# Performance work log

Measured on AMD Instinct MI355X. Metric: run time of the kernel, lower is better.

Reference implementation:

```python
import jax, jax.numpy as jnp
import numpy as np

N = 50000      # nodes
E = 600000     # edges
DIN = 128
H1, H2, H3 = 128, 128, 64
EPS = 1e-5


def setup_inputs() -> dict:
    key = jax.random.key(0)
    ks = jax.random.split(key, 12)
    x = jax.random.normal(ks[0], (N, DIN), jnp.float32)
    edge_index = jax.random.randint(ks[1], (2, E), 0, N, dtype=jnp.int32).astype(jnp.int64)
    s = lambda f: np.float32(1.0 / np.sqrt(f))
    W1 = jax.random.normal(ks[2], (DIN, H1), jnp.float32) * s(DIN)
    b1 = jnp.zeros((H1,), jnp.float32)
    W2 = jax.random.normal(ks[3], (H1, H2), jnp.float32) * s(H1)
    b2 = jnp.zeros((H2,), jnp.float32)
    W3 = jax.random.normal(ks[4], (H2, H3), jnp.float32) * s(H2)
    b3 = jnp.zeros((H3,), jnp.float32)
    g1 = 1.0 + 0.1 * jax.random.normal(ks[5], (H1,), jnp.float32)
    be1 = 0.1 * jax.random.normal(ks[6], (H1,), jnp.float32)
    g2 = 1.0 + 0.1 * jax.random.normal(ks[7], (H2,), jnp.float32)
    be2 = 0.1 * jax.random.normal(ks[8], (H2,), jnp.float32)
    return {"x": x, "edge_index": edge_index, "W1": W1, "b1": b1, "g1": g1,
            "be1": be1, "W2": W2, "b2": b2, "g2": g2, "be2": be2,
            "W3": W3, "b3": b3}


def _gcn(h_in, W, b, src_sl, dst_sl, norm, n):
    # GCNConv: h = X W; out_i = sum_{j->i} norm_ij * h_j + b  (self-loops included)
    h = h_in @ W
    msg = h[src_sl] * norm[:, None]          # [E+N, F] gather + scale
    out = jax.ops.segment_sum(msg, dst_sl, num_segments=n)
    return out + b


def _bn(x, g, b):
    # training-mode BatchNorm1d over nodes (biased variance, eps=1e-5)
    m = x.mean(0)
    v = x.var(0)
    return g * (x - m) * jax.lax.rsqrt(v + EPS) + b


def reference(x, edge_index, W1, b1, g1, be1, W2, b2, g2, be2, W3, b3):
    src, dst = edge_index[0], edge_index[1]
    loops = jnp.arange(N, dtype=src.dtype)
    src_sl = jnp.concatenate([src, loops])
    dst_sl = jnp.concatenate([dst, loops])
    deg = jax.ops.segment_sum(jnp.ones_like(dst_sl, jnp.float32), dst_sl,
                              num_segments=N)
    dinv = jnp.where(deg > 0, jax.lax.rsqrt(deg), 0.0)
    norm = dinv[src_sl] * dinv[dst_sl]       # symmetric D^-1/2 (A+I) D^-1/2

    h = _gcn(x, W1, b1, src_sl, dst_sl, norm, N)
    h = jax.nn.relu(_bn(h, g1, be1))         # dropout is identity in eval mode
    h = _gcn(h, W2, b2, src_sl, dst_sl, norm, N)
    h = jax.nn.relu(_bn(h, g2, be2))
    out = _gcn(h, W3, b3, src_sl, dst_sl, norm, N)  # [N, 64]
    return out
```

## Files before the change

kernel.cpp:

```cpp
#include <hip/hip_runtime.h>
#include <hip/hip_bf16.h>


typedef __attribute__((ext_vector_type(8))) short short8;
typedef __attribute__((ext_vector_type(4))) float f32x4;

__device__ inline unsigned short f2bf(float f) {
    unsigned int u = __float_as_uint(f);
    return (unsigned short)((u + 0x7fff + ((u >> 16) & 1)) >> 16);
}
__device__ inline float bf2f_lo(unsigned int p) { return __uint_as_float(p << 16); }
__device__ inline float bf2f_hi(unsigned int p) { return __uint_as_float(p & 0xffff0000u); }

__device__ inline void bf4_acc(uint2 v, float* a) {
    a[0] += bf2f_lo(v.x); a[1] += bf2f_hi(v.x);
    a[2] += bf2f_lo(v.y); a[3] += bf2f_hi(v.y);
}

__global__ void prep_kernel(const int* __restrict__ dst, int E,
                            int* __restrict__ deg,
                            const float* __restrict__ x,
                            unsigned short* __restrict__ xb, int total4,
                            const float* __restrict__ W1,
                            const float* __restrict__ W2,
                            const float* __restrict__ W3,
                            unsigned short* __restrict__ wt1,
                            unsigned short* __restrict__ wt2,
                            unsigned short* __restrict__ wt3,
                            int EB, int XB) {
    const int b = blockIdx.x;
    const int t = threadIdx.x;
    if (b < EB) {
        int e = b * 256 + t;
        if (e < E) atomicAdd(deg + dst[e], 1);
    } else if (b < EB + XB) {
        int i = (b - EB) * 256 + t;
        if (i < total4) {
            float4 v = reinterpret_cast<const float4*>(x)[i];
            uint2 p;
            p.x = f2bf(v.x) | ((unsigned)f2bf(v.y) << 16);
            p.y = f2bf(v.z) | ((unsigned)f2bf(v.w) << 16);
            reinterpret_cast<uint2*>(xb)[i] = p;
        }
    } else if (b < EB + XB + 64) {
        int idx = (b - EB - XB) * 256 + t;
        int k = idx >> 7, nn = idx & 127;
        wt1[nn * 128 + k] = f2bf(W1[idx]);
    } else if (b < EB + XB + 128) {
        int idx = (b - EB - XB - 64) * 256 + t;
        int k = idx >> 7, nn = idx & 127;
        wt2[nn * 128 + k] = f2bf(W2[idx]);
    } else {
        int idx = (b - EB - XB - 128) * 256 + t;
        int k = idx >> 6, nn = idx & 63;
        wt3[nn * 128 + k] = f2bf(W3[idx]);
    }
}

__global__ __launch_bounds__(256) void prescan_kernel(
    const int* __restrict__ deg, int n, int B, float* __restrict__ dinv,
    int* __restrict__ bh, int* __restrict__ rowptr, int* __restrict__ bsum) {
    __shared__ int lh[64];
    __shared__ int sh[256];
    const int t = threadIdx.x, b = blockIdx.x;
    if (t < 64) lh[t] = 0;
    __syncthreads();
    const int base = b * 2048 + t * 8;
    int v[8];
    int run = 0;
#pragma unroll
    for (int j = 0; j < 8; ++j) {
        int idx = base + j;
        int d = 0;
        if (idx < n) {
            d = deg[idx];
            dinv[idx] = rsqrtf((float)(d + 1));
            atomicAdd(&lh[min(d, 63)], 1);
        }
        run += d;
        v[j] = run;
    }
    sh[t] = run;
    __syncthreads();
#pragma unroll
    for (int off = 1; off < 256; off <<= 1) {
        int add = (t >= off) ? sh[t - off] : 0;
        __syncthreads();
        sh[t] += add;
        __syncthreads();
    }
    int prev = (t > 0) ? sh[t - 1] : 0;
#pragma unroll
    for (int j = 0; j < 8; ++j) {
        int idx = base + j;
        if (idx < n) rowptr[idx + 1] = v[j] + prev;
    }
    if (t == 255) bsum[b] = sh[255];
    if (b == 0 && t == 0) rowptr[0] = 0;
    if (t < 64) bh[t * B + b] = lh[t];
}

__global__ void midscan_kernel(int* __restrict__ bh, int totalbh,
                               int* __restrict__ bsum, int B) {
    __shared__ int sh[256];
    const int t = threadIdx.x;
    int base = 0;
    for (int start = 0; start < totalbh; start += 256) {
        int i = start + t;
        int v = (i < totalbh) ? bh[i] : 0;
        sh[t] = v;
        __syncthreads();
#pragma unroll
        for (int off = 1; off < 256; off <<= 1) {
            int add = (t >= off) ? sh[t - off] : 0;
            __syncthreads();
            sh[t] += add;
            __syncthreads();
        }
        int excl = (t > 0 ? sh[t - 1] : 0) + base;
        if (i < totalbh) bh[i] = excl;
        base += sh[255];
        __syncthreads();
    }
    int v = (t < B) ? bsum[t] : 0;
    sh[t] = v;
    __syncthreads();
#pragma unroll
    for (int off = 1; off < 64; off <<= 1) {
        int add = (t >= off && t < 64) ? sh[t - off] : 0;
        __syncthreads();
        if (t < 64) sh[t] += add;
        __syncthreads();
    }
    if (t < B) bsum[t] = sh[t];
}

__global__ void place_scanC_kernel(const int* __restrict__ deg, int n, int B,
                                   const int* __restrict__ bh,
                                   const int* __restrict__ bsum,
                                   int* __restrict__ perm,
                                   int* __restrict__ rowptr) {
    const int t = threadIdx.x;
    if ((int)blockIdx.x < B) {
        const int b = blockIdx.x;
        __shared__ int lbase[64];
        __shared__ int lcur[64];
        if (t < 64) {
            lbase[t] = bh[t * B + b];
            lcur[t] = 0;
        }
        __syncthreads();
        const int lim = min((b + 1) * 2048, n);
        for (int i = b * 2048 + t; i < lim; i += 256) {
            int d = min(deg[i], 63);
            int r = atomicAdd(&lcur[d], 1);
            perm[lbase[d] + r] = i;
        }
    } else {
        const int c = blockIdx.x - B;
        if (c == 0) return;
        const int off = bsum[c - 1];
        const int lim = min((c + 1) * 2048, n);
        for (int i = c * 2048 + t; i < lim; i += 256) rowptr[i + 1] += off;
    }
}

__global__ void csr_build_kernel(const int* __restrict__ src,
                                 const int* __restrict__ dst, int E,
                                 int* __restrict__ rowptr,
                                 int* __restrict__ csr_src) {
    int e = blockIdx.x * blockDim.x + threadIdx.x;
    if (e < E) {
        int pos = atomicAdd(rowptr + dst[e], 1);
        csr_src[pos] = src[e];
    }
}

template <int NC, bool BN>
__global__ __launch_bounds__(256) void gemm_mfma(
    const unsigned short* __restrict__ A, const unsigned short* __restrict__ Wt,
    unsigned short* __restrict__ C, int n, const float* __restrict__ stats,
    const float* __restrict__ g, const float* __restrict__ be, float invn,
    const float* __restrict__ dinv) {
    __shared__ unsigned short Asd[64][136];
    __shared__ unsigned short Bsd[64][136];
    __shared__ float ssl[256];
    const int tid = threadIdx.x;
    const int wave = tid >> 6;
    const int lane = tid & 63;
    const int row0 = blockIdx.x * 64;
    const int col0 = blockIdx.y * 64;

    if (BN) {
        if (tid < 128) {
            float mean = stats[tid] * invn;
            float var = fmaf(-mean, mean, stats[128 + tid] * invn);
            float sc = g[tid] * rsqrtf(var + 1e-5f);
            ssl[tid] = sc;
            ssl[128 + tid] = fmaf(-mean, sc, be[tid]);
        }
        __syncthreads();
    }

    for (int idx = tid; idx < 64 * 16; idx += 256) {
        int r = idx >> 4;
        int c = (idx & 15) * 8;
        uint4 v = *reinterpret_cast<const uint4*>(Wt + (size_t)(col0 + r) * 128 + c);
        *reinterpret_cast<uint4*>(&Bsd[r][c]) = v;
    }
    for (int idx = tid; idx < 64 * 16; idx += 256) {
        int r = idx >> 4;
        int c = (idx & 15) * 8;
        int grow = row0 + r;
        uint4 v = make_uint4(0u, 0u, 0u, 0u);
        if (grow < n)
            v = *reinterpret_cast<const uint4*>(A + (size_t)grow * 128 + c);
        if (BN) {
            unsigned int p[4] = {v.x, v.y, v.z, v.w};
#pragma unroll
            for (int h = 0; h < 4; ++h) {
                int f = c + h * 2;
                float lo = fmaxf(fmaf(bf2f_lo(p[h]), ssl[f], ssl[128 + f]), 0.f);
                float hi = fmaxf(fmaf(bf2f_hi(p[h]), ssl[f + 1], ssl[129 + f]), 0.f);
                p[h] = f2bf(lo) | ((unsigned)f2bf(hi) << 16);
            }
            v = make_uint4(p[0], p[1], p[2], p[3]);
        }
        *reinterpret_cast<uint4*>(&Asd[r][c]) = v;
    }
    __syncthreads();

    f32x4 acc[4];
#pragma unroll
    for (int t = 0; t < 4; ++t) acc[t] = (f32x4)(0.f);

    const int l15 = lane & 15;
    const int quad = lane >> 4;
#pragma unroll
    for (int kb = 0; kb < 128; kb += 32) {
        short8 a = *reinterpret_cast<const short8*>(&Asd[wave * 16 + l15][kb + quad * 8]);
#pragma unroll
        for (int t = 0; t < 4; ++t) {
            short8 b = *reinterpret_cast<const short8*>(&Bsd[t * 16 + l15][kb + quad * 8]);
            acc[t] = __builtin_amdgcn_mfma_f32_16x16x32_bf16(a, b, acc[t], 0, 0, 0);
        }
    }

    const int rbase = row0 + wave * 16 + quad * 4;
    float dv[4] = {0.f, 0.f, 0.f, 0.f};
    if (rbase < n) {
        float4 d4 = *reinterpret_cast<const float4*>(dinv + rbase);
        dv[0] = d4.x; dv[1] = d4.y; dv[2] = d4.z; dv[3] = d4.w;
    }
#pragma unroll
    for (int t = 0; t < 4; ++t) {
        int col = col0 + t * 16 + l15;
#pragma unroll
        for (int r = 0; r < 4; ++r) {
            int row = rbase + r;
            if (row < n)
                C[(size_t)row * NC + col] = f2bf(acc[t][r] * dv[r]);
        }
    }
}

template <int F, bool STATS, bool OBF, bool SPLIT>
__global__ __launch_bounds__(256) void aggregate_kernel(
    const unsigned short* __restrict__ hs, const int* __restrict__ csr_src,
    const int* __restrict__ rowptr, const int* __restrict__ perm,
    const float* __restrict__ dinv, const float* __restrict__ bias,
    void* __restrict__ outp, int n, float* __restrict__ stats) {
    constexpr int FH = SPLIT ? (F / 2) : F;
    constexpr int LANES = FH / 4;
    constexpr int GROUPS = 256 / LANES;
    int wb = blockIdx.x;
    int nw = gridDim.x;
    int hb = 0;
    if (SPLIT) {
        const int xcd = wb & 7;
        hb = (xcd >= 4) ? (F / 2) : 0;
        wb = (wb >> 3) * 4 + (xcd & 3);
        nw = (nw >> 3) * 4;
    }
    const int lane = threadIdx.x % LANES;
    const int grp = threadIdx.x / LANES;
    const int fq = hb + lane * 4;
    const float4 b4 = *reinterpret_cast<const float4*>(bias + fq);
    float s[4] = {}, sq[4] = {};

    const int stride = nw * GROUPS * 4;

    for (int j0 = (wb * GROUPS + grp) * 4; j0 < n; j0 += stride) {
        const int nv = min(4, n - j0);
        int nd[4], e[4], end[4];
        float acc[4][4] = {};
#pragma unroll
        for (int q = 0; q < 4; ++q) {
            if (q < nv) {
                int node = perm[j0 + q];
                nd[q] = node;
                e[q] = (node == 0) ? 0 : rowptr[node - 1];
                end[q] = rowptr[node];
            } else {
                nd[q] = -1; e[q] = 0; end[q] = 0;
            }
        }
#pragma unroll
        for (int q = 0; q < 4; ++q)
            if (nd[q] >= 0)
                bf4_acc(*reinterpret_cast<const uint2*>(hs + (size_t)nd[q] * F + fq), acc[q]);
        int rem = end[0] - e[0];
#pragma unroll
        for (int q = 1; q < 4; ++q)
            if (q < nv) rem = min(rem, end[q] - e[q]);
        for (; rem >= 2; rem -= 2) {
            int i0[4], i1[4];
#pragma unroll
            for (int q = 0; q < 4; ++q) {
                i0[q] = csr_src[e[q]];
                i1[q] = csr_src[e[q] + 1];
                e[q] += 2;
            }
            uint2 v0[4], v1[4];
#pragma unroll
            for (int q = 0; q < 4; ++q) {
                v0[q] = *reinterpret_cast<const uint2*>(hs + (size_t)i0[q] * F + fq);
                v1[q] = *reinterpret_cast<const uint2*>(hs + (size_t)i1[q] * F + fq);
            }
#pragma unroll
            for (int q = 0; q < 4; ++q) {
                bf4_acc(v0[q], acc[q]);
                bf4_acc(v1[q], acc[q]);
            }
        }
#pragma unroll
        for (int q = 0; q < 4; ++q) {
            for (; e[q] < end[q]; ++e[q]) {
                int s0 = csr_src[e[q]];
                bf4_acc(*reinterpret_cast<const uint2*>(hs + (size_t)s0 * F + fq), acc[q]);
            }
        }
#pragma unroll
        for (int q = 0; q < 4; ++q) {
            if (nd[q] < 0) continue;
            const float di = dinv[nd[q]];
            float y[4];
            y[0] = fmaf(di, acc[q][0], b4.x);
            y[1] = fmaf(di, acc[q][1], b4.y);
            y[2] = fmaf(di, acc[q][2], b4.z);
            y[3] = fmaf(di, acc[q][3], b4.w);
            if (OBF) {
                uint2 p;
                p.x = f2bf(y[0]) | ((unsigned)f2bf(y[1]) << 16);
                p.y = f2bf(y[2]) | ((unsigned)f2bf(y[3]) << 16);
                *reinterpret_cast<uint2*>((unsigned short*)outp + (size_t)nd[q] * F + fq) = p;
            } else {
                *reinterpret_cast<float4*>((float*)outp + (size_t)nd[q] * F + fq) =
                    make_float4(y[0], y[1], y[2], y[3]);
            }
            if (STATS) {
#pragma unroll
                for (int j = 0; j < 4; ++j) {
                    s[j] += y[j];
                    sq[j] = fmaf(y[j], y[j], sq[j]);
                }
            }
        }
    }

    if (STATS) {
        __shared__ float sred[LANES][GROUPS + 1];
#pragma unroll
        for (int q = 0; q < 8; ++q) {
            float v = (q < 4) ? s[q] : sq[q - 4];
            sred[lane][grp] = v;
            __syncthreads();
            if (grp == 0) {
                float t = 0.f;
#pragma unroll
                for (int g = 0; g < GROUPS; ++g) t += sred[lane][g];
                int f = fq + (q & 3);
                atomicAdd(stats + ((q < 4) ? f : 128 + f), t);
            }
            __syncthreads();
        }
    }
}

extern "C" void kernel_launch(void* const* d_in, const int* in_sizes, int n_in,
                              void* d_out, int out_size, void* d_ws,
                              size_t ws_size, hipStream_t stream) {
    const float* x   = (const float*)d_in[0];
    const int*   ei  = (const int*)d_in[1];
    const float* W1  = (const float*)d_in[2];
    const float* b1  = (const float*)d_in[3];
    const float* g1  = (const float*)d_in[4];
    const float* be1 = (const float*)d_in[5];
    const float* W2  = (const float*)d_in[6];
    const float* b2  = (const float*)d_in[7];
    const float* g2  = (const float*)d_in[8];
    const float* be2 = (const float*)d_in[9];
    const float* W3  = (const float*)d_in[10];
    const float* b3  = (const float*)d_in[11];
    float* out = (float*)d_out;

    const int n = in_sizes[0] / 128;
    const int E = in_sizes[1] / 2;
    const int* src = ei;
    const int* dst = ei + E;

    const int B = (n + 2047) / 2048;

    float* wsf    = (float*)d_ws;
    float* stats1 = wsf;
    float* stats2 = stats1 + 256;
    int*   deg    = (int*)(stats2 + 256);
    float* dinv   = (float*)(deg + n);
    int*   bh     = (int*)(dinv + n + 64);
    int*   bsum   = bh + 64 * 32;
    int*   rowptr = bsum + 64;
    int*   perm   = rowptr + (n + 1);
    int*   csrsrc = perm + n;
    unsigned short* wt1 = (unsigned short*)(csrsrc + E);
    unsigned short* wt2 = wt1 + 128 * 128;
    unsigned short* wt3 = wt2 + 128 * 128;
    unsigned short* abuf = wt3 + 64 * 128;
    unsigned short* hsb  = abuf + (size_t)n * 128;

    const int EB = (E + 255) / 256;
    const int total4 = n * 32;
    const int XB = (total4 + 255) / 256;

    hipMemsetAsync(wsf, 0, (size_t)(512 + n) * 4, stream);
    prep_kernel<<<EB + XB + 160, 256, 0, stream>>>(dst, E, deg, x, abuf, total4,
                                                   W1, W2, W3, wt1, wt2, wt3,
                                                   EB, XB);
    prescan_kernel<<<B, 256, 0, stream>>>(deg, n, B, dinv, bh, rowptr, bsum);
    midscan_kernel<<<1, 256, 0, stream>>>(bh, 64 * B, bsum, B);
    place_scanC_kernel<<<2 * B, 256, 0, stream>>>(deg, n, B, bh, bsum, perm, rowptr);
    csr_build_kernel<<<EB, 256, 0, stream>>>(src, dst, E, rowptr, csrsrc);

    const int gemmRows = (n + 63) / 64;
    dim3 gemmGrid128(gemmRows, 2);
    dim3 gemmGrid64(gemmRows, 1);
    const int aggGrid = 512;
    const float invn = 1.0f / n;

    gemm_mfma<128, false><<<gemmGrid128, 256, 0, stream>>>(abuf, wt1, hsb, n, nullptr, nullptr, nullptr, invn, dinv);
    aggregate_kernel<128, true, true, true><<<aggGrid, 256, 0, stream>>>(hsb, csrsrc, rowptr, perm, dinv, b1, abuf, n, stats1);
    gemm_mfma<128, true><<<gemmGrid128, 256, 0, stream>>>(abuf, wt2, hsb, n, stats1, g1, be1, invn, dinv);
    aggregate_kernel<128, true, true, true><<<aggGrid, 256, 0, stream>>>(hsb, csrsrc, rowptr, perm, dinv, b2, abuf, n, stats2);
    gemm_mfma<64, true><<<gemmGrid64, 256, 0, stream>>>(abuf, wt3, hsb, n, stats2, g2, be2, invn, dinv);
    aggregate_kernel<64, false, false, false><<<aggGrid, 256, 0, stream>>>(hsb, csrsrc, rowptr, perm, dinv, b3, out, n, nullptr);
}
```

Before: 393.8 us.

## Partition CSR edges by source quarter and aggregate in grid-synchronized phases

Edges are bucketed per destination node by which quarter of the node range their source falls in, which builds a 4×-granular rowptr. The aggregation kernel then walks the four source quarters in separate phases separated by a software grid barrier. The aim is to keep each phase's gathered feature rows (about a quarter of the hidden matrix) resident in L2 and raise cache hit rates on the random gathers. In exchange it adds three grid-wide spin barriers per aggregation, which rely on all 512 blocks being co-resident. It also fixes a per-thread node count (MAXB=4) that only covers graphs up to a certain size, and makes the CSR build scans four times larger.

```diff
diff --git a/kernel.cpp b/kernel.cpp
--- a/kernel.cpp
+++ b/kernel.cpp
@@ -17,8 +17,9 @@
     a[2] += bf2f_lo(v.y); a[3] += bf2f_hi(v.y);
 }
 
-__global__ void prep_kernel(const int* __restrict__ dst, int E,
-                            int* __restrict__ deg,
+__global__ void prep_kernel(const int* __restrict__ src,
+                            const int* __restrict__ dst, int E, int qs,
+                            int* __restrict__ bc,
                             const float* __restrict__ x,
                             unsigned short* __restrict__ xb, int total4,
                             const float* __restrict__ W1,
@@ -32,7 +33,11 @@
     const int t = threadIdx.x;
     if (b < EB) {
         int e = b * 256 + t;
-        if (e < E) atomicAdd(deg + dst[e], 1);
+        if (e < E) {
+            int q = src[e] / qs;
+            if (q > 3) q = 3;
+            atomicAdd(bc + dst[e] * 4 + q, 1);
+        }
     } else if (b < EB + XB) {
         int i = (b - EB) * 256 + t;
         if (i < total4) {
@@ -57,28 +62,37 @@
     }
 }
 
-__global__ __launch_bounds__(256) void prescan_kernel(
-    const int* __restrict__ deg, int n, int B, float* __restrict__ dinv,
-    int* __restrict__ bh, int* __restrict__ rowptr, int* __restrict__ bsum) {
+__global__ __launch_bounds__(256) void prescan4_kernel(
+    const int* __restrict__ bc, int n, int B4, int* __restrict__ deg,
+    float* __restrict__ dinv, int* __restrict__ bh,
+    int* __restrict__ rowptr4, int* __restrict__ bsum4) {
     __shared__ int lh[64];
     __shared__ int sh[256];
     const int t = threadIdx.x, b = blockIdx.x;
+    const int n4 = n * 4;
     if (t < 64) lh[t] = 0;
     __syncthreads();
     const int base = b * 2048 + t * 8;
+    int c[8];
     int v[8];
     int run = 0;
 #pragma unroll
     for (int j = 0; j < 8; ++j) {
         int idx = base + j;
-        int d = 0;
-        if (idx < n) {
-            d = deg[idx];
-            dinv[idx] = rsqrtf((float)(d + 1));
+        c[j] = (idx < n4) ? bc[idx] : 0;
+        run += c[j];
+        v[j] = run;
+    }
+    const int node0 = base >> 2;
+#pragma unroll
+    for (int m = 0; m < 2; ++m) {
+        int node = node0 + m;
+        if (node < n) {
+            int d = c[m * 4] + c[m * 4 + 1] + c[m * 4 + 2] + c[m * 4 + 3];
+            deg[node] = d;
+            dinv[node] = rsqrtf((float)(d + 1));
             atomicAdd(&lh[min(d, 63)], 1);
         }
-        run += d;
-        v[j] = run;
     }
     sh[t] = run;
     __syncthreads();
@@ -93,15 +107,15 @@
 #pragma unroll
     for (int j = 0; j < 8; ++j) {
         int idx = base + j;
-        if (idx < n) rowptr[idx + 1] = v[j] + prev;
-    }
-    if (t == 255) bsum[b] = sh[255];
-    if (b == 0 && t == 0) rowptr[0] = 0;
-    if (t < 64) bh[t * B + b] = lh[t];
-}
-
-__global__ void midscan_kernel(int* __restrict__ bh, int totalbh,
-                               int* __restrict__ bsum, int B) {
+        if (idx < n4) rowptr4[idx + 1] = v[j] + prev;
+    }
+    if (t == 255) bsum4[b] = sh[255];
+    if (b == 0 && t == 0) rowptr4[0] = 0;
+    if (t < 64) bh[t * B4 + b] = lh[t];
+}
+
+__global__ void midscan4_kernel(int* __restrict__ bh, int totalbh,
+                                int* __restrict__ bsum4, int B4) {
     __shared__ int sh[256];
     const int t = threadIdx.x;
     int base = 0;
@@ -122,57 +136,232 @@
         base += sh[255];
         __syncthreads();
     }
-    int v = (t < B) ? bsum[t] : 0;
+    int v = (t < B4) ? bsum4[t] : 0;
     sh[t] = v;
     __syncthreads();
 #pragma unroll
-    for (int off = 1; off < 64; off <<= 1) {
-        int add = (t >= off && t < 64) ? sh[t - off] : 0;
-        __syncthreads();
-        if (t < 64) sh[t] += add;
-        __syncthreads();
-    }
-    if (t < B) bsum[t] = sh[t];
-}
-
-__global__ void place_scanC_kernel(const int* __restrict__ deg, int n, int B,
-                                   const int* __restrict__ bh,
-                                   const int* __restrict__ bsum,
-                                   int* __restrict__ perm,
-                                   int* __restrict__ rowptr) {
+    for (int off = 1; off < 256; off <<= 1) {
+        int add = (t >= off) ? sh[t - off] : 0;
+        __syncthreads();
+        sh[t] += add;
+        __syncthreads();
+    }
+    if (t < B4) bsum4[t] = sh[t];
+}
+
+__global__ void place_scanC4_kernel(const int* __restrict__ deg, int n, int B4,
+                                    const int* __restrict__ bh,
+                                    const int* __restrict__ bsum4,
+                                    int* __restrict__ perm,
+                                    int* __restrict__ rowptr4) {
     const int t = threadIdx.x;
-    if ((int)blockIdx.x < B) {
+    if ((int)blockIdx.x < B4) {
         const int b = blockIdx.x;
         __shared__ int lbase[64];
         __shared__ int lcur[64];
         if (t < 64) {
-            lbase[t] = bh[t * B + b];
+            lbase[t] = bh[t * B4 + b];
             lcur[t] = 0;
         }
         __syncthreads();
-        const int lim = min((b + 1) * 2048, n);
-        for (int i = b * 2048 + t; i < lim; i += 256) {
+        const int lim = min((b + 1) * 512, n);
+        for (int i = b * 512 + t; i < lim; i += 256) {
             int d = min(deg[i], 63);
             int r = atomicAdd(&lcur[d], 1);
             perm[lbase[d] + r] = i;
         }
     } else {
-        const int c = blockIdx.x - B;
+        const int c = blockIdx.x - B4;
         if (c == 0) return;
-        const int off = bsum[c - 1];
-        const int lim = min((c + 1) * 2048, n);
-        for (int i = c * 2048 + t; i < lim; i += 256) rowptr[i + 1] += off;
-    }
-}
-
-__global__ void csr_build_kernel(const int* __restrict__ src,
-                                 const int* __restrict__ dst, int E,
-                                 int* __restrict__ rowptr,
-                                 int* __restrict__ csr_src) {
+        const int off = bsum4[c - 1];
+        const int n4 = n * 4;
+        const int lim = min((c + 1) * 2048, n4);
+        for (int i = c * 2048 + t; i < lim; i += 256) rowptr4[i + 1] += off;
+    }
+}
+
+__global__ void csr_build4_kernel(const int* __restrict__ src,
+                                  const int* __restrict__ dst, int E, int qs,
+                                  int* __restrict__ rowptr4,
+                                  int* __restrict__ csr_src) {
     int e = blockIdx.x * blockDim.x + threadIdx.x;
     if (e < E) {
-        int pos = atomicAdd(rowptr + dst[e], 1);
-        csr_src[pos] = src[e];
+        int s = src[e];
+        int q = s / qs;
+        if (q > 3) q = 3;
+        int pos = atomicAdd(rowptr4 + dst[e] * 4 + q, 1);
+        csr_src[pos] = s;
+    }
+}
+
+__device__ inline void gbar(int* bar, int target) {
+    __syncthreads();
+    if (threadIdx.x == 0) {
+        atomicAdd(bar, 1);
+        int spins = 0;
+        while (__hip_atomic_load(bar, __ATOMIC_RELAXED,
+                                 __HIP_MEMORY_SCOPE_AGENT) < target &&
+               spins < (1 << 16)) {
+            __builtin_amdgcn_s_sleep(8);
+            ++spins;
+        }
+    }
+    __syncthreads();
+}
+
+template <int F, bool STATS, bool OBF, bool SPLIT>
+__global__ __launch_bounds__(256) void aggregate4_kernel(
+    const unsigned short* __restrict__ hs, const int* __restrict__ csr_src,
+    const int* __restrict__ rowptr4, const int* __restrict__ perm,
+    const float* __restrict__ dinv, const float* __restrict__ bias,
+    void* __restrict__ outp, int n, int qs, float* __restrict__ stats,
+    int* __restrict__ bar) {
+    constexpr int FH = SPLIT ? (F / 2) : F;
+    constexpr int LANES = FH / 4;
+    constexpr int GROUPS = 256 / LANES;
+    constexpr int MAXB = 4;
+    int wb = blockIdx.x;
+    int nw = gridDim.x;
+    const int nb = gridDim.x;
+    int hb = 0;
+    if (SPLIT) {
+        const int xcd = wb & 7;
+        hb = (xcd >= 4) ? (F / 2) : 0;
+        wb = (wb >> 3) * 4 + (xcd & 3);
+        nw = (nw >> 3) * 4;
+    }
+    const int lane = threadIdx.x % LANES;
+    const int grp = threadIdx.x / LANES;
+    const int fq = hb + lane * 4;
+    const float4 b4 = *reinterpret_cast<const float4*>(bias + fq);
+    float s[4] = {}, sq[4] = {};
+
+    const int stride = nw * GROUPS * 4;
+    const int j00 = (wb * GROUPS + grp) * 4;
+
+    int nd[MAXB][4];
+    int qsel[MAXB][4];
+    float acc[MAXB][4][4] = {};
+
+#pragma unroll
+    for (int bt = 0; bt < MAXB; ++bt) {
+        const int j0 = j00 + bt * stride;
+#pragma unroll
+        for (int q = 0; q < 4; ++q) {
+            if (j0 + q < n) {
+                int node = perm[j0 + q];
+                nd[bt][q] = node;
+                int qv = node / qs;
+                qsel[bt][q] = (qv > 3) ? 3 : qv;
+            } else {
+                nd[bt][q] = -1;
+                qsel[bt][q] = -1;
+            }
+        }
+    }
+
+    for (int p = 0; p < 4; ++p) {
+#pragma unroll
+        for (int bt = 0; bt < MAXB; ++bt) {
+            int e[4], end[4];
+#pragma unroll
+            for (int q = 0; q < 4; ++q) {
+                if (nd[bt][q] >= 0) {
+                    int k = nd[bt][q] * 4 + p;
+                    e[q] = (k == 0) ? 0 : rowptr4[k - 1];
+                    end[q] = rowptr4[k];
+                    if (qsel[bt][q] == p)
+                        bf4_acc(*reinterpret_cast<const uint2*>(
+                                    hs + (size_t)nd[bt][q] * F + fq),
+                                acc[bt][q]);
+                } else {
+                    e[q] = 0;
+                    end[q] = 0;
+                }
+            }
+            int rem = end[0] - e[0];
+#pragma unroll
+            for (int q = 1; q < 4; ++q)
+                if (nd[bt][q] >= 0) rem = min(rem, end[q] - e[q]);
+            for (; rem >= 2; rem -= 2) {
+                int i0[4], i1[4];
+#pragma unroll
+                for (int q = 0; q < 4; ++q) {
+                    i0[q] = csr_src[e[q]];
+                    i1[q] = csr_src[e[q] + 1];
+                    e[q] += 2;
+                }
+                uint2 v0[4], v1[4];
+#pragma unroll
+                for (int q = 0; q < 4; ++q) {
+                    v0[q] = *reinterpret_cast<const uint2*>(hs + (size_t)i0[q] * F + fq);
+                    v1[q] = *reinterpret_cast<const uint2*>(hs + (size_t)i1[q] * F + fq);
+                }
+#pragma unroll
+                for (int q = 0; q < 4; ++q) {
+                    bf4_acc(v0[q], acc[bt][q]);
+                    bf4_acc(v1[q], acc[bt][q]);
+                }
+            }
+#pragma unroll
+            for (int q = 0; q < 4; ++q) {
+                for (; e[q] < end[q]; ++e[q]) {
+                    int s0 = csr_src[e[q]];
+                    bf4_acc(*reinterpret_cast<const uint2*>(hs + (size_t)s0 * F + fq),
+                            acc[bt][q]);
+                }
+            }
+        }
+        if (p < 3) gbar(bar, nb * (p + 1));
+    }
+
+#pragma unroll
+    for (int bt = 0; bt < MAXB; ++bt) {
+#pragma unroll
+        for (int q = 0; q < 4; ++q) {
+            if (nd[bt][q] < 0) continue;
+            const float di = dinv[nd[bt][q]];
+            float y[4];
+            y[0] = fmaf(di, acc[bt][q][0], b4.x);
+            y[1] = fmaf(di, acc[bt][q][1], b4.y);
+            y[2] = fmaf(di, acc[bt][q][2], b4.z);
+            y[3] = fmaf(di, acc[bt][q][3], b4.w);
+            if (OBF) {
+                uint2 p2;
+                p2.x = f2bf(y[0]) | ((unsigned)f2bf(y[1]) << 16);
+                p2.y = f2bf(y[2]) | ((unsigned)f2bf(y[3]) << 16);
+                *reinterpret_cast<uint2*>((unsigned short*)outp +
+                                          (size_t)nd[bt][q] * F + fq) = p2;
+            } else {
+                *reinterpret_cast<float4*>((float*)outp + (size_t)nd[bt][q] * F + fq) =
+                    make_float4(y[0], y[1], y[2], y[3]);
+            }
+            if (STATS) {
+#pragma unroll
+                for (int j = 0; j < 4; ++j) {
+                    s[j] += y[j];
+                    sq[j] = fmaf(y[j], y[j], sq[j]);
+                }
+            }
+        }
+    }
+
+    if (STATS) {
+        __shared__ float sred[LANES][GROUPS + 1];
+#pragma unroll
+        for (int q = 0; q < 8; ++q) {
+            float v = (q < 4) ? s[q] : sq[q - 4];
+            sred[lane][grp] = v;
+            __syncthreads();
+            if (grp == 0) {
+                float t2 = 0.f;
+#pragma unroll
+                for (int g = 0; g < GROUPS; ++g) t2 += sred[lane][g];
+                int f = fq + (q & 3);
+                atomicAdd(stats + ((q < 4) ? f : 128 + f), t2);
+            }
+            __syncthreads();
+        }
     }
 }
 
@@ -260,129 +449,6 @@
             int row = rbase + r;
             if (row < n)
                 C[(size_t)row * NC + col] = f2bf(acc[t][r] * dv[r]);
-        }
-    }
-}
-
-template <int F, bool STATS, bool OBF, bool SPLIT>
-__global__ __launch_bounds__(256) void aggregate_kernel(
-    const unsigned short* __restrict__ hs, const int* __restrict__ csr_src,
-    const int* __restrict__ rowptr, const int* __restrict__ perm,
-    const float* __restrict__ dinv, const float* __restrict__ bias,
-    void* __restrict__ outp, int n, float* __restrict__ stats) {
-    constexpr int FH = SPLIT ? (F / 2) : F;
-    constexpr int LANES = FH / 4;
-    constexpr int GROUPS = 256 / LANES;
-    int wb = blockIdx.x;
-    int nw = gridDim.x;
-    int hb = 0;
-    if (SPLIT) {
-        const int xcd = wb & 7;
-        hb = (xcd >= 4) ? (F / 2) : 0;
-        wb = (wb >> 3) * 4 + (xcd & 3);
-        nw = (nw >> 3) * 4;
-    }
-    const int lane = threadIdx.x % LANES;
-    const int grp = threadIdx.x / LANES;
-    const int fq = hb + lane * 4;
-    const float4 b4 = *reinterpret_cast<const float4*>(bias + fq);
-    float s[4] = {}, sq[4] = {};
-
-    const int stride = nw * GROUPS * 4;
-
-    for (int j0 = (wb * GROUPS + grp) * 4; j0 < n; j0 += stride) {
-        const int nv = min(4, n - j0);
-        int nd[4], e[4], end[4];
-        float acc[4][4] = {};
-#pragma unroll
-        for (int q = 0; q < 4; ++q) {
-            if (q < nv) {
-                int node = perm[j0 + q];
-                nd[q] = node;
-                e[q] = (node == 0) ? 0 : rowptr[node - 1];
-                end[q] = rowptr[node];
-            } else {
-                nd[q] = -1; e[q] = 0; end[q] = 0;
-            }
-        }
-#pragma unroll
-        for (int q = 0; q < 4; ++q)
-            if (nd[q] >= 0)
-                bf4_acc(*reinterpret_cast<const uint2*>(hs + (size_t)nd[q] * F + fq), acc[q]);
-        int rem = end[0] - e[0];
-#pragma unroll
-        for (int q = 1; q < 4; ++q)
-            if (q < nv) rem = min(rem, end[q] - e[q]);
-        for (; rem >= 2; rem -= 2) {
-            int i0[4], i1[4];
-#pragma unroll
-            for (int q = 0; q < 4; ++q) {
-                i0[q] = csr_src[e[q]];
-                i1[q] = csr_src[e[q] + 1];
-                e[q] += 2;
-            }
-            uint2 v0[4], v1[4];
-#pragma unroll
-            for (int q = 0; q < 4; ++q) {
-                v0[q] = *reinterpret_cast<const uint2*>(hs + (size_t)i0[q] * F + fq);
-                v1[q] = *reinterpret_cast<const uint2*>(hs + (size_t)i1[q] * F + fq);
-            }
-#pragma unroll
-            for (int q = 0; q < 4; ++q) {
-                bf4_acc(v0[q], acc[q]);
-                bf4_acc(v1[q], acc[q]);
-            }
-        }
-#pragma unroll
-        for (int q = 0; q < 4; ++q) {
-            for (; e[q] < end[q]; ++e[q]) {
-                int s0 = csr_src[e[q]];
-                bf4_acc(*reinterpret_cast<const uint2*>(hs + (size_t)s0 * F + fq), acc[q]);
-            }
-        }
-#pragma unroll
-        for (int q = 0; q < 4; ++q) {
-            if (nd[q] < 0) continue;
-            const float di = dinv[nd[q]];
-            float y[4];
-            y[0] = fmaf(di, acc[q][0], b4.x);
-            y[1] = fmaf(di, acc[q][1], b4.y);
-            y[2] = fmaf(di, acc[q][2], b4.z);
-            y[3] = fmaf(di, acc[q][3], b4.w);
-            if (OBF) {
-                uint2 p;
-                p.x = f2bf(y[0]) | ((unsigned)f2bf(y[1]) << 16);
-                p.y = f2bf(y[2]) | ((unsigned)f2bf(y[3]) << 16);
-                *reinterpret_cast<uint2*>((unsigned short*)outp + (size_t)nd[q] * F + fq) = p;
-            } else {
-                *reinterpret_cast<float4*>((float*)outp + (size_t)nd[q] * F + fq) =
-                    make_float4(y[0], y[1], y[2], y[3]);
-            }
-            if (STATS) {
-#pragma unroll
-                for (int j = 0; j < 4; ++j) {
-                    s[j] += y[j];
-                    sq[j] = fmaf(y[j], y[j], sq[j]);
-                }
-            }
-        }
-    }
-
-    if (STATS) {
-        __shared__ float sred[LANES][GROUPS + 1];
-#pragma unroll
-        for (int q = 0; q < 8; ++q) {
-            float v = (q < 4) ? s[q] : sq[q - 4];
-            sred[lane][grp] = v;
-            __syncthreads();
-            if (grp == 0) {
-                float t = 0.f;
-#pragma unroll
-                for (int g = 0; g < GROUPS; ++g) t += sred[lane][g];
-                int f = fq + (q & 3);
-                atomicAdd(stats + ((q < 4) ? f : 128 + f), t);
-            }
-            __syncthreads();
         }
     }
 }
@@ -409,17 +475,27 @@
     const int* src = ei;
     const int* dst = ei + E;
 
-    const int B = (n + 2047) / 2048;
+    const int qs = (n + 3) / 4;
+    const int B4 = (4 * n + 2047) / 2048;
+    const int EB = (E + 255) / 256;
+    const int total4 = n * 32;
+    const int XB = (total4 + 255) / 256;
+    const int gemmRows = (n + 63) / 64;
+    dim3 gemmGrid128(gemmRows, 2);
+    dim3 gemmGrid64(gemmRows, 1);
+    const float invn = 1.0f / n;
 
     float* wsf    = (float*)d_ws;
     float* stats1 = wsf;
     float* stats2 = stats1 + 256;
-    int*   deg    = (int*)(stats2 + 256);
+    int*   barr   = (int*)(stats2 + 256);
+    int*   bc     = barr + 8;
+    int*   deg    = bc + 4 * n;
     float* dinv   = (float*)(deg + n);
     int*   bh     = (int*)(dinv + n + 64);
-    int*   bsum   = bh + 64 * 32;
-    int*   rowptr = bsum + 64;
-    int*   perm   = rowptr + (n + 1);
+    int*   bsum4  = bh + 64 * 128;
+    int*   rowptr4= bsum4 + 256;
+    int*   perm   = rowptr4 + 4 * n + 4;
     int*   csrsrc = perm + n;
     unsigned short* wt1 = (unsigned short*)(csrsrc + E);
     unsigned short* wt2 = wt1 + 128 * 128;
@@ -427,29 +503,27 @@
     unsigned short* abuf = wt3 + 64 * 128;
     unsigned short* hsb  = abuf + (size_t)n * 128;
 
-    const int EB = (E + 255) / 256;
-    const int total4 = n * 32;
-    const int XB = (total4 + 255) / 256;
-
-    hipMemsetAsync(wsf, 0, (size_t)(512 + n) * 4, stream);
-    prep_kernel<<<EB + XB + 160, 256, 0, stream>>>(dst, E, deg, x, abuf, total4,
+    hipMemsetAsync(wsf, 0, (size_t)(512 + 8 + 4 * n) * 4, stream);
+    prep_kernel<<<EB + XB + 160, 256, 0, stream>>>(src, dst, E, qs, bc,
+                                                   x, abuf, total4,
                                                    W1, W2, W3, wt1, wt2, wt3,
                                                    EB, XB);
-    prescan_kernel<<<B, 256, 0, stream>>>(deg, n, B, dinv, bh, rowptr, bsum);
-    midscan_kernel<<<1, 256, 0, stream>>>(bh, 64 * B, bsum, B);
-    place_scanC_kernel<<<2 * B, 256, 0, stream>>>(deg, n, B, bh, bsum, perm, rowptr);
-    csr_build_kernel<<<EB, 256, 0, stream>>>(src, dst, E, rowptr, csrsrc);
-
-    const int gemmRows = (n + 63) / 64;
-    dim3 gemmGrid128(gemmRows, 2);
-    dim3 gemmGrid64(gemmRows, 1);
+    prescan4_kernel<<<B4, 256, 0, stream>>>(bc, n, B4, deg, dinv, bh, rowptr4, bsum4);
+    midscan4_kernel<<<1, 256, 0, stream>>>(bh, 64 * B4, bsum4, B4);
+    place_scanC4_kernel<<<2 * B4, 256, 0, stream>>>(deg, n, B4, bh, bsum4, perm, rowptr4);
+    csr_build4_kernel<<<EB, 256, 0, stream>>>(src, dst, E, qs, rowptr4, csrsrc);
+
     const int aggGrid = 512;
-    const float invn = 1.0f / n;
-
-    gemm_mfma<128, false><<<gemmGrid128, 256, 0, stream>>>(abuf, wt1, hsb, n, nullptr, nullptr, nullptr, invn, dinv);
-    aggregate_kernel<128, true, true, true><<<aggGrid, 256, 0, stream>>>(hsb, csrsrc, rowptr, perm, dinv, b1, abuf, n, stats1);
-    gemm_mfma<128, true><<<gemmGrid128, 256, 0, stream>>>(abuf, wt2, hsb, n, stats1, g1, be1, invn, dinv);
-    aggregate_kernel<128, true, true, true><<<aggGrid, 256, 0, stream>>>(hsb, csrsrc, rowptr, perm, dinv, b2, abuf, n, stats2);
-    gemm_mfma<64, true><<<gemmGrid64, 256, 0, stream>>>(abuf, wt3, hsb, n, stats2, g2, be2, invn, dinv);
-    aggregate_kernel<64, false, false, false><<<aggGrid, 256, 0, stream>>>(hsb, csrsrc, rowptr, perm, dinv, b3, out, n, nullptr);
-}
+    gemm_mfma<128, false><<<gemmGrid128, 256, 0, stream>>>(
+        abuf, wt1, hsb, n, nullptr, nullptr, nullptr, invn, dinv);
+    aggregate4_kernel<128, true, true, true><<<aggGrid, 256, 0, stream>>>(
+        hsb, csrsrc, rowptr4, perm, dinv, b1, abuf, n, qs, stats1, barr + 0);
+    gemm_mfma<128, true><<<gemmGrid128, 256, 0, stream>>>(
+        abuf, wt2, hsb, n, stats1, g1, be1, invn, dinv);
+    aggregate4_kernel<128, true, true, true><<<aggGrid, 256, 0, stream>>>(
+        hsb, csrsrc, rowptr4, perm, dinv, b2, abuf, n, qs, stats2, barr + 1);
+    gemm_mfma<64, true><<<gemmGrid64, 256, 0, stream>>>(
+        abuf, wt3, hsb, n, stats2, g2, be2, invn, dinv);
+    aggregate4_kernel<64, false, false, false><<<aggGrid, 256, 0, stream>>>(
+        hsb, csrsrc, rowptr4, perm, dinv, b3, out, n, qs, nullptr, barr + 2);
+}
```

Result: slower. 856.3 us (+117.5%).
